# Optimization experiments

Hardware: AMD Instinct MI355X
Metric: run time of the kernel (lower is better)

## Reference

```python
import jax, jax.numpy as jnp
import numpy as np

B, S, D = 2, 2048, 1024
H = 16
HD = D // H

def setup_inputs() -> dict:
    key = jax.random.key(0)
    ks = jax.random.split(key, 9)
    s = 1.0 / np.sqrt(D)
    return {
        "x": jax.random.normal(ks[0], (B, S, D), dtype=jnp.float32),
        "Wq": jax.random.normal(ks[1], (D, D), dtype=jnp.float32) * s,
        "bq": jnp.zeros((D,), dtype=jnp.float32),
        "Wk": jax.random.normal(ks[2], (D, D), dtype=jnp.float32) * s,
        "bk": jnp.zeros((D,), dtype=jnp.float32),
        "Wv": jax.random.normal(ks[3], (D, D), dtype=jnp.float32) * s,
        "bv": jnp.zeros((D,), dtype=jnp.float32),
        "Wo": jax.random.normal(ks[4], (D, D), dtype=jnp.float32) * s,
        "bo": jnp.zeros((D,), dtype=jnp.float32),
    }

def reference(x, Wq, bq, Wk, bk, Wv, bv, Wo, bo):
    b, s, d = x.shape
    # torch Linear: y = x @ W.T + b
    def proj(W, bias):
        y = jnp.einsum('bsd,ed->bse', x, W) + bias
        return y.reshape(b, s, H, HD).transpose(0, 2, 1, 3)  # [b,h,s,hd]
    Q = proj(Wq, bq)
    K = proj(Wk, bk)
    V = proj(Wv, bv)
    scale = 1.0 / jnp.sqrt(jnp.float32(HD))
    scores = jnp.einsum('bhqd,bhkd->bhqk', Q, K) * scale  # [b,h,s,s]
    attn = jax.nn.softmax(scores, axis=-1)
    out = jnp.einsum('bhqk,bhkd->bhqd', attn, V)  # [b,h,s,hd]
    out = out.transpose(0, 2, 1, 3).reshape(b, s, d)
    return jnp.einsum('bsd,ed->bse', out, Wo) + bo
```

## Files before the change

### kernel.cpp

```cpp
#include <hip/hip_runtime.h>
#include <stdint.h>


typedef __bf16 bf16x8 __attribute__((ext_vector_type(8)));
typedef float  f32x4  __attribute__((ext_vector_type(4)));

#define LOG2E 1.44269504088896f
#define FIXED_MAX_BITS 14.4269504088896f

__device__ __forceinline__ unsigned short f2bf(float f) {
    union { float f; unsigned u; } v; v.f = f;
    unsigned r = v.u + 0x7FFFu + ((v.u >> 16) & 1u);
    return (unsigned short)(r >> 16);
}

__device__ __forceinline__ float exp2_fast(float x) {
#if __has_builtin(__builtin_amdgcn_exp2f)
    return __builtin_amdgcn_exp2f(x);
#else
    return __expf(x * 0.69314718056f);
#endif
}

__device__ __forceinline__ void glds16(const void* g, void* l) {
    __builtin_amdgcn_global_load_lds(
        (__attribute__((address_space(1))) void*)(g),
        (__attribute__((address_space(3))) void*)(l),
        16, 0, 0);
}

__global__ __launch_bounds__(256) void cvt_all(
    const float* __restrict__ x,  const float* __restrict__ Wq,
    const float* __restrict__ Wk, const float* __restrict__ Wv,
    const float* __restrict__ Wo,
    unsigned short* __restrict__ xb,  unsigned short* __restrict__ Wqb,
    unsigned short* __restrict__ Wkb, unsigned short* __restrict__ Wvb,
    unsigned short* __restrict__ Wob)
{
    const int stride = gridDim.x * blockDim.x;
    for (int i = blockIdx.x * blockDim.x + threadIdx.x; i < 2097152; i += stride) {
        const float* src; unsigned short* dst; int j;
        if (i < 1048576) { src = x; dst = xb; j = i; }
        else {
            int t = (i - 1048576) >> 18; j = (i - 1048576) & 262143;
            src = (t == 0) ? Wq : (t == 1) ? Wk : (t == 2) ? Wv : Wo;
            dst = (t == 0) ? Wqb : (t == 1) ? Wkb : (t == 2) ? Wvb : Wob;
        }
        float4 v = ((const float4*)src)[j];
        ushort4 o;
        o.x = f2bf(v.x); o.y = f2bf(v.y); o.z = f2bf(v.z); o.w = f2bf(v.w);
        ((ushort4*)dst)[j] = o;
    }
}

template <int MODE>
__global__ __launch_bounds__(256) void gemm_bt(
    const unsigned short* __restrict__ A,
    const unsigned short* __restrict__ W0,
    const unsigned short* __restrict__ W1,
    const unsigned short* __restrict__ W2,
    const float* __restrict__ b0,
    const float* __restrict__ b1,
    const float* __restrict__ b2,
    unsigned short* __restrict__ outQ,
    unsigned short* __restrict__ outK,
    unsigned short* __restrict__ outV,
    float* __restrict__ outF)
{
    constexpr int BM = (MODE == 0) ? 128 : 64;
    constexpr int FM = BM / 32;
    constexpr int RA = BM / 32;

    __shared__ __attribute__((aligned(16))) unsigned short As[BM * 64];
    __shared__ __attribute__((aligned(16))) unsigned short Bs[128 * 64];

    const int tid  = threadIdx.x;
    const int lane = tid & 63;
    const int wid  = tid >> 6;
    const int quad = lane >> 4;
    const int l16  = lane & 15;

    const int m0 = blockIdx.x * BM;

    const unsigned short* W;
    const float* bias;
    int proj, n0;
    if (MODE == 0) {
        proj = blockIdx.y >> 3;
        n0   = (blockIdx.y & 7) * 128;
        W    = (proj == 0) ? W0 : (proj == 1) ? W1 : W2;
        bias = (proj == 0) ? b0 : (proj == 1) ? b1 : b2;
    } else {
        proj = 0;
        n0   = blockIdx.y * 128;
        W    = W0;
        bias = b0;
    }

    const int wm = (wid >> 1) * (BM / 2);
    const int wn = (wid & 1) * 64;

    f32x4 acc[FM][4];
#pragma unroll
    for (int i = 0; i < FM; ++i)
#pragma unroll
        for (int j = 0; j < 4; ++j)
            acc[i][j] = (f32x4){0.f, 0.f, 0.f, 0.f};

    char* AsB  = (char*)As;
    char* BsB  = (char*)Bs;
    char* ldsA = AsB + wid * 1024;
    char* ldsB = BsB + wid * 1024;

    for (int k0 = 0; k0 < 1024; k0 += 64) {
#pragma unroll
        for (int q = 0; q < RA; ++q) {
            int i   = q * 256 + tid;
            int row = i >> 3;
            int sc  = (i & 7) ^ (row & 7);
            glds16(A + (size_t)(m0 + row) * 1024 + k0 + sc * 8, ldsA + q * 4096);
        }
#pragma unroll
        for (int q = 0; q < 4; ++q) {
            int i   = q * 256 + tid;
            int row = i >> 3;
            int sc  = (i & 7) ^ (row & 7);
            glds16(W + (size_t)(n0 + row) * 1024 + k0 + sc * 8, ldsB + q * 4096);
        }
        __syncthreads();

#pragma unroll
        for (int kh = 0; kh < 2; ++kh) {
            bf16x8 af[FM], bfr[4];
#pragma unroll
            for (int t = 0; t < FM; ++t) {
                int r = wm + t * 16 + l16;
                int c = (kh * 4 + quad) ^ (r & 7);
                af[t] = *(const bf16x8*)(AsB + r * 128 + c * 16);
            }
#pragma unroll
            for (int t = 0; t < 4; ++t) {
                int r = wn + t * 16 + l16;
                int c = (kh * 4 + quad) ^ (r & 7);
                bfr[t] = *(const bf16x8*)(BsB + r * 128 + c * 16);
            }
#pragma unroll
            for (int i = 0; i < FM; ++i)
#pragma unroll
                for (int j = 0; j < 4; ++j)
                    acc[i][j] = __builtin_amdgcn_mfma_f32_16x16x32_bf16(
                        af[i], bfr[j], acc[i][j], 0, 0, 0);
        }
        __syncthreads();
    }

#pragma unroll
    for (int i = 0; i < FM; ++i) {
        const int mrow0 = m0 + wm + i * 16 + quad * 4;
#pragma unroll
        for (int j = 0; j < 4; ++j) {
            const int n  = n0 + wn + j * 16 + l16;
            const float bb = bias[n];
            if (MODE == 1) {
#pragma unroll
                for (int r = 0; r < 4; ++r)
                    outF[(size_t)(mrow0 + r) * 1024 + n] = acc[i][j][r] + bb;
            } else {
                const int h = n >> 6, hd = n & 63;
                if (proj == 2) {
                    const int b = mrow0 >> 11, s = mrow0 & 2047;
                    ushort4 pk;
                    pk.x = f2bf(acc[i][j][0] + bb);
                    pk.y = f2bf(acc[i][j][1] + bb);
                    pk.z = f2bf(acc[i][j][2] + bb);
                    pk.w = f2bf(acc[i][j][3] + bb);
                    *(ushort4*)(outV + ((size_t)((b * 16 + h) * 64 + hd)) * 2048 + s) = pk;
                } else {
                    unsigned short* dst = (proj == 0) ? outQ : outK;
                    const float scl = (proj == 0) ? (0.125f * LOG2E) : 1.0f;
#pragma unroll
                    for (int r = 0; r < 4; ++r) {
                        const int m = mrow0 + r;
                        const int b = m >> 11, s = m & 2047;
                        dst[((size_t)((b * 16 + h) * 2048 + s)) * 64 + hd] =
                            f2bf((acc[i][j][r] + bb) * scl);
                    }
                }
            }
        }
    }
}

__global__ __launch_bounds__(256) void attn_kernel(
    const unsigned short* __restrict__ Qb,
    const unsigned short* __restrict__ Kb,
    const unsigned short* __restrict__ Vtb,
    unsigned short* __restrict__ Ob)
{
    __shared__ __attribute__((aligned(16))) unsigned short Ks[128 * 64];
    __shared__ __attribute__((aligned(16))) unsigned short Vs[2 * 64 * 64];
    __shared__ __attribute__((aligned(16))) unsigned short Ps[4][16 * 64];

    const int tid  = threadIdx.x;
    const int lane = tid & 63;
    const int wid  = tid >> 6;
    const int quad = lane >> 4;
    const int l16  = lane & 15;

    const int q0 = blockIdx.x * 64;
    const int hb = blockIdx.y;
    const int bq = hb >> 4, hh = hb & 15;

    const unsigned short* Qh  = Qb  + (size_t)hb * 2048 * 64;
    const unsigned short* Kh  = Kb  + (size_t)hb * 2048 * 64;
    const unsigned short* Vth = Vtb + (size_t)hb * 64 * 2048;

    const int mq = q0 + wid * 16 + l16;
    const unsigned short* qp = Qh + (size_t)mq * 64 + quad * 8;
    const bf16x8 aq0 = *(const bf16x8*)(qp);
    const bf16x8 aq1 = *(const bf16x8*)(qp + 32);

    f32x4 o[4];
#pragma unroll
    for (int t = 0; t < 4; ++t) o[t] = (f32x4){0.f, 0.f, 0.f, 0.f};
    float lsum[4] = {0.f, 0.f, 0.f, 0.f};

    char* KsB = (char*)Ks;
    unsigned short* Pw = Ps[wid];
    char* ldsK = KsB + wid * 1024;

    for (int kc = 0; kc < 2048; kc += 128) {
#pragma unroll
        for (int q = 0; q < 4; ++q) {
            int i   = q * 256 + tid;
            int row = i >> 3;
            int sc  = (i & 7) ^ (row & 7);
            glds16(Kh + (size_t)(kc + row) * 64 + sc * 8, ldsK + q * 4096);
        }
#pragma unroll
        for (int sub = 0; sub < 2; ++sub)
#pragma unroll
            for (int q = 0; q < 2; ++q) {
                int i   = q * 256 + tid;
                int row = i >> 3;
                int sc  = (i & 7) ^ (row & 7);
                glds16(Vth + (size_t)row * 2048 + kc + sub * 64 + sc * 8,
                       (char*)Vs + sub * 8192 + wid * 1024 + q * 4096);
            }
        __syncthreads();

#pragma unroll
        for (int ss = 0; ss < 2; ++ss) {
            char* VsB = (char*)Vs + ss * 8192;

            f32x4 p[4];
#pragma unroll
            for (int nt = 0; nt < 4; ++nt) {
                const int srow = ss * 64 + nt * 16 + l16;
                const int c0 = quad ^ (srow & 7);
                const int c1 = (4 + quad) ^ (srow & 7);
                bf16x8 k0 = *(const bf16x8*)(KsB + srow * 128 + c0 * 16);
                bf16x8 k1 = *(const bf16x8*)(KsB + srow * 128 + c1 * 16);
                f32x4 t = (f32x4){-FIXED_MAX_BITS, -FIXED_MAX_BITS,
                                  -FIXED_MAX_BITS, -FIXED_MAX_BITS};
                t = __builtin_amdgcn_mfma_f32_16x16x32_bf16(aq0, k0, t, 0, 0, 0);
                t = __builtin_amdgcn_mfma_f32_16x16x32_bf16(aq1, k1, t, 0, 0, 0);
                p[nt] = t;
            }
#pragma unroll
            for (int nt = 0; nt < 4; ++nt)
#pragma unroll
                for (int r = 0; r < 4; ++r)
                    p[nt][r] = exp2_fast(p[nt][r]);
#pragma unroll
            for (int r = 0; r < 4; ++r)
                lsum[r] += (p[0][r] + p[1][r]) + (p[2][r] + p[3][r]);

#pragma unroll
            for (int nt = 0; nt < 4; ++nt) {
                const int col = nt * 16 + l16;
                const int cch = col >> 3, cin = col & 7;
#pragma unroll
                for (int r = 0; r < 4; ++r) {
                    const int m = quad * 4 + r;
                    Pw[m * 64 + ((cch ^ (m & 7)) << 3) + cin] = f2bf(p[nt][r]);
                }
            }
            bf16x8 ap0, ap1;
            {
                const int m  = l16;
                const int c0 = quad ^ (m & 7);
                const int c1 = (4 + quad) ^ (m & 7);
                ap0 = *(const bf16x8*)((char*)Pw + m * 128 + c0 * 16);
                ap1 = *(const bf16x8*)((char*)Pw + m * 128 + c1 * 16);
            }

#pragma unroll
            for (int ot = 0; ot < 4; ++ot) {
                const int n  = ot * 16 + l16;
                const int c0 = quad ^ (n & 7);
                const int c1 = (4 + quad) ^ (n & 7);
                bf16x8 v0 = *(const bf16x8*)(VsB + n * 128 + c0 * 16);
                bf16x8 v1 = *(const bf16x8*)(VsB + n * 128 + c1 * 16);
                o[ot] = __builtin_amdgcn_mfma_f32_16x16x32_bf16(ap0, v0, o[ot], 0, 0, 0);
                o[ot] = __builtin_amdgcn_mfma_f32_16x16x32_bf16(ap1, v1, o[ot], 0, 0, 0);
            }
        }
        __syncthreads();
    }

    float rl[4];
#pragma unroll
    for (int r = 0; r < 4; ++r) {
        float s = lsum[r];
        s += __shfl_xor(s, 1);
        s += __shfl_xor(s, 2);
        s += __shfl_xor(s, 4);
        s += __shfl_xor(s, 8);
        rl[r] = 1.0f / s;
    }
#pragma unroll
    for (int ot = 0; ot < 4; ++ot) {
        const int hd = ot * 16 + l16;
#pragma unroll
        for (int r = 0; r < 4; ++r) {
            const int m = q0 + wid * 16 + quad * 4 + r;
            Ob[(size_t)(bq * 2048 + m) * 1024 + hh * 64 + hd] = f2bf(o[ot][r] * rl[r]);
        }
    }
}

extern "C" void kernel_launch(void* const* d_in, const int* in_sizes, int n_in,
                              void* d_out, int out_size, void* d_ws, size_t ws_size,
                              hipStream_t stream) {
    (void)in_sizes; (void)n_in; (void)out_size; (void)ws_size;

    const float* x  = (const float*)d_in[0];
    const float* Wq = (const float*)d_in[1];
    const float* bq = (const float*)d_in[2];
    const float* Wk = (const float*)d_in[3];
    const float* bk = (const float*)d_in[4];
    const float* Wv = (const float*)d_in[5];
    const float* bv = (const float*)d_in[6];
    const float* Wo = (const float*)d_in[7];
    const float* bo = (const float*)d_in[8];

    char* ws = (char*)d_ws;
    const size_t MB = 1024 * 1024;
    unsigned short* xb    = (unsigned short*)(ws + 0);
    unsigned short* Wqb   = (unsigned short*)(ws + 8  * MB);
    unsigned short* Wkb   = (unsigned short*)(ws + 10 * MB);
    unsigned short* Wvb   = (unsigned short*)(ws + 12 * MB);
    unsigned short* Wob   = (unsigned short*)(ws + 14 * MB);
    unsigned short* Qb    = (unsigned short*)(ws + 16 * MB);
    unsigned short* Kb    = (unsigned short*)(ws + 24 * MB);
    unsigned short* Vtb   = (unsigned short*)(ws + 32 * MB);
    unsigned short* attnb = (unsigned short*)(ws + 40 * MB);

    cvt_all<<<dim3(1024), dim3(256), 0, stream>>>(
        x, Wq, Wk, Wv, Wo, xb, Wqb, Wkb, Wvb, Wob);

    gemm_bt<0><<<dim3(32, 24), dim3(256), 0, stream>>>(
        xb, Wqb, Wkb, Wvb, bq, bk, bv, Qb, Kb, Vtb, nullptr);

    attn_kernel<<<dim3(32, 32), dim3(256), 0, stream>>>(Qb, Kb, Vtb, attnb);

    gemm_bt<1><<<dim3(64, 8), dim3(256), 0, stream>>>(
        attnb, Wob, nullptr, nullptr, bo, nullptr, nullptr,
        nullptr, nullptr, nullptr, (float*)d_out);
}
```

Baseline: 210.4 us.

## Prefetch next K/V tile into registers instead of direct global-to-LDS loads

Replaces the direct global-to-LDS copies of each K and V chunk with register staging. The next chunk is loaded into registers right after the barrier, so its memory latency overlaps with the MFMA and softmax work on the current chunk. Launch bounds also ask for 4 blocks per SM. The cost is 8 extra float4 registers per thread and an extra register-to-LDS store pass, and the occupancy hint may force register spills.

```diff
diff --git a/kernel.cpp b/kernel.cpp
--- a/kernel.cpp
+++ b/kernel.cpp
@@ -191,7 +191,7 @@
     }
 }
 
-__global__ __launch_bounds__(256) void attn_kernel(
+__global__ __launch_bounds__(256, 4) void attn_kernel(
     const unsigned short* __restrict__ Qb,
     const unsigned short* __restrict__ Kb,
     const unsigned short* __restrict__ Vtb,
@@ -227,27 +227,52 @@
 
     char* KsB = (char*)Ks;
     unsigned short* Pw = Ps[wid];
-    char* ldsK = KsB + wid * 1024;
+
+    int krow[4], ksc[4];
+#pragma unroll
+    for (int q = 0; q < 4; ++q) {
+        int i = q * 256 + tid;
+        krow[q] = i >> 3;
+        ksc[q]  = (i & 7) ^ (krow[q] & 7);
+    }
+
+    float4 kv[8];
+
+#pragma unroll
+    for (int q = 0; q < 4; ++q)
+        kv[q] = *(const float4*)(Kh + (size_t)krow[q] * 64 + ksc[q] * 8);
+#pragma unroll
+    for (int sub = 0; sub < 2; ++sub)
+#pragma unroll
+        for (int q = 0; q < 2; ++q)
+            kv[4 + sub * 2 + q] = *(const float4*)
+                (Vth + (size_t)krow[q] * 2048 + sub * 64 + ksc[q] * 8);
 
     for (int kc = 0; kc < 2048; kc += 128) {
 #pragma unroll
-        for (int q = 0; q < 4; ++q) {
-            int i   = q * 256 + tid;
-            int row = i >> 3;
-            int sc  = (i & 7) ^ (row & 7);
-            glds16(Kh + (size_t)(kc + row) * 64 + sc * 8, ldsK + q * 4096);
-        }
+        for (int q = 0; q < 4; ++q)
+            *(float4*)(KsB + wid * 1024 + q * 4096 + lane * 16) = kv[q];
 #pragma unroll
         for (int sub = 0; sub < 2; ++sub)
 #pragma unroll
-            for (int q = 0; q < 2; ++q) {
-                int i   = q * 256 + tid;
-                int row = i >> 3;
-                int sc  = (i & 7) ^ (row & 7);
-                glds16(Vth + (size_t)row * 2048 + kc + sub * 64 + sc * 8,
-                       (char*)Vs + sub * 8192 + wid * 1024 + q * 4096);
-            }
+            for (int q = 0; q < 2; ++q)
+                *(float4*)((char*)Vs + sub * 8192 + wid * 1024 + q * 4096 + lane * 16)
+                    = kv[4 + sub * 2 + q];
         __syncthreads();
+
+        if (kc + 128 < 2048) {
+            const int kn = kc + 128;
+#pragma unroll
+            for (int q = 0; q < 4; ++q)
+                kv[q] = *(const float4*)
+                    (Kh + (size_t)(kn + krow[q]) * 64 + ksc[q] * 8);
+#pragma unroll
+            for (int sub = 0; sub < 2; ++sub)
+#pragma unroll
+                for (int q = 0; q < 2; ++q)
+                    kv[4 + sub * 2 + q] = *(const float4*)
+                        (Vth + (size_t)krow[q] * 2048 + kn + sub * 64 + ksc[q] * 8);
+        }
 
 #pragma unroll
         for (int ss = 0; ss < 2; ++ss) {
```

Result: slower. 310.2 us (+47.4%).
